# Optimization experiments

Hardware: AMD Instinct MI355X
Metric: run time of the kernel (lower is better)

The kernel has to match this reference:

```python
import jax, jax.numpy as jnp
import numpy as np

N = 25000
E = 400000
HIDDEN = 512
NH = 8
DH = HIDDEN // NH


def setup_inputs() -> dict:
    key = jax.random.key(0)
    ks = jax.random.split(key, 10)
    s = 1.0 / np.sqrt(HIDDEN)
    return {
        "h": jax.random.normal(ks[0], (N, HIDDEN), dtype=jnp.float32),
        "Wq": jax.random.normal(ks[1], (HIDDEN, HIDDEN), dtype=jnp.float32) * s,
        "bq": jnp.zeros((HIDDEN,), dtype=jnp.float32),
        "Wk": jax.random.normal(ks[2], (HIDDEN, HIDDEN), dtype=jnp.float32) * s,
        "bk": jnp.zeros((HIDDEN,), dtype=jnp.float32),
        "Wo": jax.random.normal(ks[3], (HIDDEN, HIDDEN), dtype=jnp.float32) * s,
        "bo": jnp.zeros((HIDDEN,), dtype=jnp.float32),
        "rows": jax.random.randint(ks[4], (E,), 0, N, dtype=jnp.int32),
        "cols": jax.random.randint(ks[5], (E,), 0, N, dtype=jnp.int32),
    }


def reference(h, Wq, bq, Wk, bk, Wo, bo, rows, cols):
    # Projections; reshape (N, dh, nh) exactly as the source does.
    q = (h @ Wq + bq).reshape(N, DH, NH)
    k = (h @ Wk + bk).reshape(N, DH, NH)
    v = k  # source bug kept faithfully: v = linear_k(h)

    # SDDMM: per-edge, per-head dot product (no 1/sqrt(dh) scaling in source).
    scores = jnp.einsum("edh,edh->eh", q[rows], k[cols])  # [E, NH]

    # Row-wise (source-node) segment softmax per head.
    m = jax.ops.segment_max(scores, rows, num_segments=N)       # [N, NH]
    ex = jnp.exp(scores - m[rows])                              # [E, NH]
    denom = jax.ops.segment_sum(ex, rows, num_segments=N)      # [N, NH]
    attn = ex / denom[rows]                                     # [E, NH]

    # SpMM: out[i] = sum_{j in nbr(i)} attn[ij] * v[j]
    msgs = attn[:, None, :] * v[cols]                           # [E, DH, NH]
    out = jax.ops.segment_sum(msgs, rows, num_segments=N)      # [N, DH, NH]

    return out.reshape(N, HIDDEN) @ Wo + bo
```

## Files before the change

### kernel.cpp

```cpp
#include <hip/hip_runtime.h>
#include <math.h>

typedef unsigned short u16;
typedef unsigned int u32;
typedef __attribute__((ext_vector_type(8))) _Float16 half8;
typedef __attribute__((ext_vector_type(2))) _Float16 half2v;
typedef __attribute__((ext_vector_type(8))) u16 ushort8;
typedef __attribute__((ext_vector_type(4))) float f32x4;

__device__ __forceinline__ u16 f2h(float f) {
    union { u16 u; _Float16 h; } c; c.h = (_Float16)f; return c.u;
}

#if __has_builtin(__builtin_amdgcn_fdot2)
#define FDOT2(a, b, c) __builtin_amdgcn_fdot2((a), (b), (c), false)
#else
#define FDOT2(a, b, c) fmaf((float)(a)[0], (float)(b)[0], \
                        fmaf((float)(a)[1], (float)(b)[1], (c)))
#endif

__device__ __forceinline__ void gload16(void* lds, const void* g) {
    __builtin_amdgcn_global_load_lds(
        (const __attribute__((address_space(1))) u32*)g,
        (__attribute__((address_space(3))) u32*)lds,
        16, 0, 0);
}

template <int OUTMODE>
__device__ __forceinline__ void gemm_body(
    const u16* A, const u16* Bt, const float* bias, void* Cout, int Mout,
    int m0, int n0, u16* As0, u16* As1, u16* Bs0, u16* Bs1)
{
    const int tid  = threadIdx.x;
    const int wave = tid >> 6;
    const int lane = tid & 63;
    const int wr = (wave >> 1) * 64;
    const int wc = (wave & 1) * 64;

    f32x4 acc[4][4];
#pragma unroll
    for (int i = 0; i < 4; ++i)
#pragma unroll
        for (int j = 0; j < 4; ++j) acc[i][j] = (f32x4){0.f, 0.f, 0.f, 0.f};

    const int srow  = lane >> 2;
    const int scolG = ((lane & 3) ^ ((srow >> 1) & 3)) * 8;
    const size_t gOffA = (size_t)(m0 + wave * 32 + srow) * 512 + scolG;
    const size_t gOffB = (size_t)(n0 + wave * 32 + srow) * 512 + scolG;
    const int lOff = wave * 1024 + srow * 32 + (lane & 3) * 8;

    const int fR = ((lane & 15) >> 1) & 3;
    const int paOff = (wr + (lane & 15)) * 32 + ((lane >> 4) ^ fR) * 8;
    const int pbOff = (wc + (lane & 15)) * 32 + ((lane >> 4) ^ fR) * 8;

    auto STAGE = [&](u16* sa, u16* sb, int ko) {
        gload16(sa + lOff,       A  + gOffA + ko);
        gload16(sa + lOff + 512, A  + gOffA + ko + 16 * 512);
        gload16(sb + lOff,       Bt + gOffB + ko);
        gload16(sb + lOff + 512, Bt + gOffB + ko + 16 * 512);
    };
    auto COMPUTE = [&](const u16* sa, const u16* sb) {
        half8 af[4], bf[4];
#pragma unroll
        for (int i = 0; i < 4; ++i) af[i] = *(const half8*)(sa + paOff + i * 512);
#pragma unroll
        for (int j = 0; j < 4; ++j) bf[j] = *(const half8*)(sb + pbOff + j * 512);
#pragma unroll
        for (int i = 0; i < 4; ++i)
#pragma unroll
            for (int j = 0; j < 4; ++j)
                acc[i][j] = __builtin_amdgcn_mfma_f32_16x16x32_f16(
                    af[i], bf[j], acc[i][j], 0, 0, 0);
    };

    STAGE(As0, Bs0, 0);
    __syncthreads();
#pragma unroll
    for (int kt = 0; kt < 16; kt += 2) {
        STAGE(As1, Bs1, (kt + 1) * 32);
        COMPUTE(As0, Bs0);
        __syncthreads();
        if (kt + 2 < 16) STAGE(As0, Bs0, (kt + 2) * 32);
        COMPUTE(As1, Bs1);
        __syncthreads();
    }

    const int ccol  = n0 + wc + (lane & 15);
    const int crow0 = m0 + wr + (lane >> 4) * 4;
#pragma unroll
    for (int j = 0; j < 4; ++j) {
        const float b = bias[ccol + j * 16];
#pragma unroll
        for (int i = 0; i < 4; ++i) {
#pragma unroll
            for (int r = 0; r < 4; ++r) {
                int row = crow0 + i * 16 + r;
                if (row < Mout) {
                    float v = acc[i][j][r] + b;
                    size_t off = (size_t)row * 512 + ccol + j * 16;
                    if (OUTMODE == 0) ((float*)Cout)[off] = v;
                    else              ((u16*)Cout)[off] = f2h(v);
                }
            }
        }
    }
}

__global__ __launch_bounds__(256) void gemm_qk(
    const u16* __restrict__ hh, const u16* __restrict__ Wqt,
    const u16* __restrict__ Wkt, const float* __restrict__ bqp,
    const float* __restrict__ bkp, u16* __restrict__ Qh,
    u16* __restrict__ Kb, int nPad)
{
    const int bid = blockIdx.x;
    const int m = (bid >> 6) * 8 + (bid & 7);
    const int s = (bid >> 3) & 7;
    if (m >= nPad / 128) return;
    const int z = s >> 2;
    const int n = s & 3;

    __shared__ __align__(16) u16 As0[4096], As1[4096], Bs0[4096], Bs1[4096];
    const u16* Bt = z ? Wkt : Wqt;
    const float* bias = z ? bkp : bqp;
    u16* out = z ? Kb : Qh;
    gemm_body<1>(hh, Bt, bias, out, nPad, m * 128, n * 128,
                 As0, As1, Bs0, Bs1);
}

__global__ __launch_bounds__(256) void gemm_wo(
    const u16* __restrict__ A, const u16* __restrict__ Wot,
    const float* __restrict__ bo, float* __restrict__ C, int Mout, int nPad)
{
    const int bid = blockIdx.x;
    const int m = (bid >> 5) * 8 + (bid & 7);
    const int s = (bid >> 3) & 3;
    if (m >= nPad / 128) return;

    __shared__ __align__(16) u16 As0[4096], As1[4096], Bs0[4096], Bs1[4096];
    gemm_body<0>(A, Wot, bo, C, Mout, m * 128, s * 128,
                 As0, As1, Bs0, Bs1);
}

__global__ __launch_bounds__(256) void prep(
    const float* __restrict__ h, u16* __restrict__ hh, int nN,
    const int* __restrict__ rows, int* __restrict__ deg, int E,
    const float* __restrict__ Wq, const float* __restrict__ Wk,
    const float* __restrict__ Wo, const float* __restrict__ bq,
    const float* __restrict__ bk,
    u16* __restrict__ Wqt, u16* __restrict__ Wkt, u16* __restrict__ Wot,
    float* __restrict__ bqp, float* __restrict__ bkp,
    int nbH, int nbE)
{
    __shared__ float T[64][65];
    const int tid = threadIdx.x;
    const int b = blockIdx.x;

    if (b < nbH) {
        int t = b * 256 + tid;
        size_t e = (size_t)t * 8;
        int row = (int)(e >> 9);
        ushort8 o;
        if (row < nN) {
            f32x4 a = *(const f32x4*)(h + e);
            f32x4 bb = *(const f32x4*)(h + e + 4);
            float x[8] = {a.x, a.y, a.z, a.w, bb.x, bb.y, bb.z, bb.w};
#pragma unroll
            for (int i = 0; i < 8; ++i) o[i] = f2h(x[i]);
        } else {
            o = (ushort8){0,0,0,0,0,0,0,0};
        }
        *(ushort8*)(hh + e) = o;
        return;
    }
    if (b < nbH + nbE) {
        int i = (b - nbH) * 256 + tid;
        if (i < E) atomicAdd(&deg[rows[i]], 1);
        return;
    }
    int rem = b - nbH - nbE;
    const int z = rem >> 6;
    const int X = (rem & 7) * 64;
    const int Y = ((rem >> 3) & 7) * 64;

    const int r4 = tid >> 4;
    const int c4 = (tid & 15) * 4;
    if (z < 2) {
        const float* W = z ? Wk : Wq;
#pragma unroll
        for (int rr = 0; rr < 64; rr += 16) {
            f32x4 v = *(const f32x4*)(W + (size_t)(X + rr + r4) * 512 + Y + c4);
            T[rr + r4][c4 + 0] = v.x; T[rr + r4][c4 + 1] = v.y;
            T[rr + r4][c4 + 2] = v.z; T[rr + r4][c4 + 3] = v.w;
        }
    } else {
#pragma unroll
        for (int rr = 0; rr < 64; rr += 16) {
            int p2 = (rr + r4) * 8 + (X >> 6);
            f32x4 v = *(const f32x4*)(Wo + (size_t)p2 * 512 + Y + c4);
            T[rr + r4][c4 + 0] = v.x; T[rr + r4][c4 + 1] = v.y;
            T[rr + r4][c4 + 2] = v.z; T[rr + r4][c4 + 3] = v.w;
        }
    }
    __syncthreads();

    const int cc = tid >> 2;
    const int ks = (tid & 3) * 16;
    const int pc = Y + cc;
    const int ro = (z < 2) ? ((pc & 7) * 64 + (pc >> 3)) : pc;
    ushort8 h0, h1;
#pragma unroll
    for (int t = 0; t < 8; ++t) {
        h0[t] = f2h(T[ks + t][cc]);
        h1[t] = f2h(T[ks + 8 + t][cc]);
    }
    size_t o = (size_t)ro * 512 + X + ks;
    if (z == 0) {
        *(ushort8*)(Wqt + o) = h0; *(ushort8*)(Wqt + o + 8) = h1;
    } else if (z == 1) {
        *(ushort8*)(Wkt + o) = h0; *(ushort8*)(Wkt + o + 8) = h1;
    } else {
        *(ushort8*)(Wot + o) = h0; *(ushort8*)(Wot + o + 8) = h1;
        if (rem == 128) {
            for (int bi = tid; bi < 512; bi += 256) {
                int pp = (bi & 63) * 8 + (bi >> 6);
                bqp[bi] = bq[pp];
                bkp[bi] = bk[pp];
            }
        }
    }
}

#define SCAN_CHUNK 2048

__global__ __launch_bounds__(256) void scan_partial(
    const int* __restrict__ deg, int* __restrict__ bsum, int n)
{
    int base = blockIdx.x * SCAN_CHUNK;
    int t = threadIdx.x;
    int s = 0;
    for (int i = t; i < SCAN_CHUNK; i += 256) {
        int g = base + i;
        s += (g < n) ? deg[g] : 0;
    }
#pragma unroll
    for (int off = 1; off < 64; off <<= 1) s += __shfl_xor(s, off, 64);
    __shared__ int ws[4];
    if ((t & 63) == 0) ws[t >> 6] = s;
    __syncthreads();
    if (t == 0) bsum[blockIdx.x] = ws[0] + ws[1] + ws[2] + ws[3];
}

__global__ __launch_bounds__(256) void scan_final(
    const int* __restrict__ deg, const int* __restrict__ bsum,
    int* __restrict__ rowptr, int* __restrict__ cursor, int n, int nb)
{
    int boff = 0, total = 0;
    for (int i = 0; i < nb; ++i) {
        int v = bsum[i];
        if (i < (int)blockIdx.x) boff += v;
        total += v;
    }
    int t = threadIdx.x;
    int base = blockIdx.x * SCAN_CHUNK + t * 8;
    int v[8];
    int s = 0;
#pragma unroll
    for (int i = 0; i < 8; ++i) {
        int g = base + i;
        v[i] = (g < n) ? deg[g] : 0;
        s += v[i];
    }
    int lane = t & 63, w = t >> 6;
    int inc = s;
#pragma unroll
    for (int off = 1; off < 64; off <<= 1) {
        int x = __shfl_up(inc, off, 64);
        if (lane >= off) inc += x;
    }
    __shared__ int wsum[4];
    if (lane == 63) wsum[w] = inc;
    __syncthreads();
    int excl = boff + inc - s;
    for (int i = 0; i < w; ++i) excl += wsum[i];
#pragma unroll
    for (int i = 0; i < 8; ++i) {
        int g = base + i;
        if (g < n) { rowptr[g] = excl; cursor[g] = excl; }
        excl += v[i];
    }
    if (blockIdx.x == 0 && t == 0) rowptr[n] = total;
}

__global__ void scatter_kernel(const int* __restrict__ rows, const int* __restrict__ cols,
                               int* __restrict__ cursor, int* __restrict__ colc, int E)
{
    int i = blockIdx.x * 256 + threadIdx.x;
    if (i < E) {
        int pos = atomicAdd(&cursor[rows[i]], 1);
        colc[pos] = cols[i];
    }
}

__global__ __launch_bounds__(256) void node_agg(
    const u16* __restrict__ Qh, const u16* __restrict__ Kb,
    const int* __restrict__ rowptr, const int* __restrict__ colc,
    u16* __restrict__ aggb, int nN)
{
    int node = blockIdx.x * 4 + (threadIdx.x >> 6);
    int lane = threadIdx.x & 63;
    if (node >= nN) return;
    size_t base = (size_t)node * 512 + lane * 8;

    half8 qv = __builtin_nontemporal_load((const half8*)(Qh + base));
    half2v q2[4];
#pragma unroll
    for (int i = 0; i < 4; ++i) q2[i] = (half2v){qv[2 * i], qv[2 * i + 1]};

    int start = rowptr[node];
    int deg   = rowptr[node + 1] - start;
    const int* cp = colc + start;
    const size_t loff = (size_t)lane * 8;

    float m = -__builtin_inff();
    float den = 0.f;
    half2v acc2[4];
#pragma unroll
    for (int i = 0; i < 4; ++i) acc2[i] = (half2v){(_Float16)0.f, (_Float16)0.f};

    if (deg > 0) {
        const int dl = deg - 1;
        half8 k0 = *(const half8*)(Kb + (size_t)cp[0] * 512 + loff);
        half8 k1 = *(const half8*)(Kb + (size_t)cp[1 < dl ? 1 : dl] * 512 + loff);
        half8 k2 = *(const half8*)(Kb + (size_t)cp[2 < dl ? 2 : dl] * 512 + loff);
        half8 k3 = *(const half8*)(Kb + (size_t)cp[3 < dl ? 3 : dl] * 512 + loff);
        for (int j = 0; j < deg; j += 4) {
            int i4 = j + 4 < dl ? j + 4 : dl;
            int i5 = j + 5 < dl ? j + 5 : dl;
            int i6 = j + 6 < dl ? j + 6 : dl;
            int i7 = j + 7 < dl ? j + 7 : dl;
            half8 n0 = *(const half8*)(Kb + (size_t)cp[i4] * 512 + loff);
            half8 n1 = *(const half8*)(Kb + (size_t)cp[i5] * 512 + loff);
            half8 n2 = *(const half8*)(Kb + (size_t)cp[i6] * 512 + loff);
            half8 n3 = *(const half8*)(Kb + (size_t)cp[i7] * 512 + loff);

            float p0 = 0.f, p1 = 0.f, p2 = 0.f, p3 = 0.f;
#pragma unroll
            for (int i = 0; i < 4; ++i) {
                half2v a = q2[i];
                half2v b0 = (half2v){k0[2 * i], k0[2 * i + 1]};
                half2v b1 = (half2v){k1[2 * i], k1[2 * i + 1]};
                half2v b2 = (half2v){k2[2 * i], k2[2 * i + 1]};
                half2v b3 = (half2v){k3[2 * i], k3[2 * i + 1]};
                p0 = FDOT2(a, b0, p0);
                p1 = FDOT2(a, b1, p1);
                p2 = FDOT2(a, b2, p2);
                p3 = FDOT2(a, b3, p3);
            }
#pragma unroll
            for (int off = 1; off < 8; off <<= 1) {
                p0 += __shfl_xor(p0, off, 64);
                p1 += __shfl_xor(p1, off, 64);
                p2 += __shfl_xor(p2, off, 64);
                p3 += __shfl_xor(p3, off, 64);
            }

            float pm = fmaxf(fmaxf(p0, p1), fmaxf(p2, p3));
            if (__any(pm > m + 4.f)) {
                float mn = fmaxf(m, pm);
                float sc = __expf(m - mn);
                den *= sc;
                _Float16 sch = (_Float16)sc;
                half2v sc2 = {sch, sch};
#pragma unroll
                for (int i = 0; i < 4; ++i) acc2[i] *= sc2;
                m = mn;
            }
            float w0 = __expf(p0 - m);
            float w1 = (j + 1 < deg) ? __expf(p1 - m) : 0.f;
            float w2 = (j + 2 < deg) ? __expf(p2 - m) : 0.f;
            float w3 = (j + 3 < deg) ? __expf(p3 - m) : 0.f;
            den += (w0 + w1) + (w2 + w3);
            _Float16 h0 = (_Float16)w0, h1 = (_Float16)w1;
            _Float16 h2 = (_Float16)w2, h3 = (_Float16)w3;
            half2v w02 = {h0, h0}, w12 = {h1, h1}, w22 = {h2, h2}, w32 = {h3, h3};
#pragma unroll
            for (int i = 0; i < 4; ++i) {
                half2v b0 = (half2v){k0[2 * i], k0[2 * i + 1]};
                half2v b1 = (half2v){k1[2 * i], k1[2 * i + 1]};
                half2v b2 = (half2v){k2[2 * i], k2[2 * i + 1]};
                half2v b3 = (half2v){k3[2 * i], k3[2 * i + 1]};
                acc2[i] += w02 * b0;
                acc2[i] += w12 * b1;
                acc2[i] += w22 * b2;
                acc2[i] += w32 * b3;
            }
            k0 = n0; k1 = n1; k2 = n2; k3 = n3;
        }
    }

    float inv = (deg > 0) ? 1.f / den : 0.f;
    ushort8 o;
#pragma unroll
    for (int i = 0; i < 4; ++i) {
        o[2 * i]     = f2h((float)acc2[i][0] * inv);
        o[2 * i + 1] = f2h((float)acc2[i][1] * inv);
    }
    __builtin_nontemporal_store(o, (ushort8*)(aggb + base));
}

extern "C" void kernel_launch(void* const* d_in, const int* in_sizes, int n_in,
                              void* d_out, int out_size, void* d_ws, size_t ws_size,
                              hipStream_t stream)
{
    const float* h  = (const float*)d_in[0];
    const float* Wq = (const float*)d_in[1];
    const float* bq = (const float*)d_in[2];
    const float* Wk = (const float*)d_in[3];
    const float* bk = (const float*)d_in[4];
    const float* Wo = (const float*)d_in[5];
    const float* bo = (const float*)d_in[6];
    const int* rows = (const int*)d_in[7];
    const int* cols = (const int*)d_in[8];
    float* out = (float*)d_out;

    const int HID = 512;
    const int nN  = in_sizes[0] / HID;
    const int E   = in_sizes[7];
    const int nPad = (nN + 127) & ~127;
    const int nb = (nN + SCAN_CHUNK - 1) / SCAN_CHUNK;
    const int nbH = nPad * (HID / 8) / 256;
    const int nbE = (E + 255) / 256;
    const int nMt = nPad / 128;
    const int nGrp = (nMt + 7) / 8;

    char* w = (char*)d_ws;
    u16* Kb  = (u16*)w;  w += (size_t)nPad * HID * 2;
    u16* hh  = (u16*)w;  w += (size_t)nPad * HID * 2;
    u16* Qh  = (u16*)w;  w += (size_t)nPad * HID * 2;
    u16* Wqt = (u16*)w;  w += 512 * 512 * 2;
    u16* Wkt = (u16*)w;  w += 512 * 512 * 2;
    u16* Wot = (u16*)w;  w += 512 * 512 * 2;
    float* bqp = (float*)w;  w += 512 * 4;
    float* bkp = (float*)w;  w += 512 * 4;
    int* rowptr = (int*)w;   w += (size_t)(nN + 1) * 4;
    int* cursor = (int*)w;   w += (size_t)nN * 4;
    int* deg    = (int*)w;   w += (size_t)nN * 4;
    int* bsum   = (int*)w;   w += 64 * 4;
    int* colc   = (int*)w;

    (void)hipMemsetAsync(deg, 0, (size_t)nN * sizeof(int), stream);

    prep<<<nbH + nbE + 192, 256, 0, stream>>>(
        h, hh, nN, rows, deg, E, Wq, Wk, Wo, bq, bk,
        Wqt, Wkt, Wot, bqp, bkp, nbH, nbE);

    scan_partial<<<nb, 256, 0, stream>>>(deg, bsum, nN);
    scan_final<<<nb, 256, 0, stream>>>(deg, bsum, rowptr, cursor, nN, nb);
    scatter_kernel<<<(E + 255) / 256, 256, 0, stream>>>(rows, cols, cursor, colc, E);

    gemm_qk<<<nGrp * 64, 256, 0, stream>>>(
        hh, Wqt, Wkt, bqp, bkp, Qh, Kb, nPad);

    node_agg<<<(nN + 3) / 4, 256, 0, stream>>>(Qh, Kb, rowptr, colc, hh, nN);

    gemm_wo<<<nGrp * 32, 256, 0, stream>>>(hh, Wot, bo, out, nN, nPad);
}
```

Baseline: 235.3 us.

## Widen GEMM tiles to 128x256 and deepen edge prefetch in node aggregation

The GEMM tile grows from 128x128 to 128x256 outputs per block. Each wave now holds a 4x8 MFMA accumulator, the B staging buffers double, and the grid shrinks by half. This aims to reuse A tiles across more columns and cut block count. Separately, the node aggregation loop now processes and prefetches 8 neighbor K rows per iteration instead of 4, to hide gather latency. The costs are higher register and LDS pressure, possible lower occupancy, and more wasted work for low-degree nodes.

```diff
diff --git a/kernel.cpp b/kernel.cpp
--- a/kernel.cpp
+++ b/kernel.cpp
@@ -28,47 +28,50 @@
 
 template <int OUTMODE>
 __device__ __forceinline__ void gemm_body(
-    const u16* A, const u16* Bt, const float* bias, void* Cout, int Mout,
-    int m0, int n0, u16* As0, u16* As1, u16* Bs0, u16* Bs1)
+    const u16* A, const u16* Bp, const float* bias, void* Cout, int Mout,
+    int m0, int colBase, u16* As0, u16* As1, u16* Bs0, u16* Bs1)
 {
     const int tid  = threadIdx.x;
     const int wave = tid >> 6;
     const int lane = tid & 63;
     const int wr = (wave >> 1) * 64;
-    const int wc = (wave & 1) * 64;
-
-    f32x4 acc[4][4];
+    const int wc = (wave & 1) * 128;
+
+    f32x4 acc[4][8];
 #pragma unroll
     for (int i = 0; i < 4; ++i)
 #pragma unroll
-        for (int j = 0; j < 4; ++j) acc[i][j] = (f32x4){0.f, 0.f, 0.f, 0.f};
+        for (int j = 0; j < 8; ++j) acc[i][j] = (f32x4){0.f, 0.f, 0.f, 0.f};
 
     const int srow  = lane >> 2;
     const int scolG = ((lane & 3) ^ ((srow >> 1) & 3)) * 8;
     const size_t gOffA = (size_t)(m0 + wave * 32 + srow) * 512 + scolG;
-    const size_t gOffB = (size_t)(n0 + wave * 32 + srow) * 512 + scolG;
-    const int lOff = wave * 1024 + srow * 32 + (lane & 3) * 8;
+    const size_t gOffB = (size_t)(wave * 64 + srow) * 512 + scolG;
+    const int lOffA = wave * 1024 + srow * 32 + (lane & 3) * 8;
+    const int lOffB = wave * 2048 + srow * 32 + (lane & 3) * 8;
 
     const int fR = ((lane & 15) >> 1) & 3;
     const int paOff = (wr + (lane & 15)) * 32 + ((lane >> 4) ^ fR) * 8;
     const int pbOff = (wc + (lane & 15)) * 32 + ((lane >> 4) ^ fR) * 8;
 
     auto STAGE = [&](u16* sa, u16* sb, int ko) {
-        gload16(sa + lOff,       A  + gOffA + ko);
-        gload16(sa + lOff + 512, A  + gOffA + ko + 16 * 512);
-        gload16(sb + lOff,       Bt + gOffB + ko);
-        gload16(sb + lOff + 512, Bt + gOffB + ko + 16 * 512);
+        gload16(sa + lOffA,        A  + gOffA + ko);
+        gload16(sa + lOffA + 512,  A  + gOffA + ko + 16 * 512);
+        gload16(sb + lOffB,        Bp + gOffB + ko);
+        gload16(sb + lOffB + 512,  Bp + gOffB + ko + 16 * 512);
+        gload16(sb + lOffB + 1024, Bp + gOffB + ko + 32 * 512);
+        gload16(sb + lOffB + 1536, Bp + gOffB + ko + 48 * 512);
     };
     auto COMPUTE = [&](const u16* sa, const u16* sb) {
-        half8 af[4], bf[4];
+        half8 af[4], bf[8];
 #pragma unroll
         for (int i = 0; i < 4; ++i) af[i] = *(const half8*)(sa + paOff + i * 512);
 #pragma unroll
-        for (int j = 0; j < 4; ++j) bf[j] = *(const half8*)(sb + pbOff + j * 512);
+        for (int j = 0; j < 8; ++j) bf[j] = *(const half8*)(sb + pbOff + j * 512);
 #pragma unroll
         for (int i = 0; i < 4; ++i)
 #pragma unroll
-            for (int j = 0; j < 4; ++j)
+            for (int j = 0; j < 8; ++j)
                 acc[i][j] = __builtin_amdgcn_mfma_f32_16x16x32_f16(
                     af[i], bf[j], acc[i][j], 0, 0, 0);
     };
@@ -85,11 +88,12 @@
         __syncthreads();
     }
 
-    const int ccol  = n0 + wc + (lane & 15);
+    const int ccolL = wc + (lane & 15);
     const int crow0 = m0 + wr + (lane >> 4) * 4;
 #pragma unroll
-    for (int j = 0; j < 4; ++j) {
-        const float b = bias[ccol + j * 16];
+    for (int j = 0; j < 8; ++j) {
+        const float b = bias[ccolL + j * 16];
+        const int col = colBase + ccolL + j * 16;
 #pragma unroll
         for (int i = 0; i < 4; ++i) {
 #pragma unroll
@@ -97,7 +101,7 @@
                 int row = crow0 + i * 16 + r;
                 if (row < Mout) {
                     float v = acc[i][j][r] + b;
-                    size_t off = (size_t)row * 512 + ccol + j * 16;
+                    size_t off = (size_t)row * 512 + col;
                     if (OUTMODE == 0) ((float*)Cout)[off] = v;
                     else              ((u16*)Cout)[off] = f2h(v);
                 }
@@ -113,18 +117,17 @@
     u16* __restrict__ Kb, int nPad)
 {
     const int bid = blockIdx.x;
-    const int m = (bid >> 6) * 8 + (bid & 7);
-    const int s = (bid >> 3) & 7;
+    const int m = (bid >> 5) * 8 + (bid & 7);
+    const int s = (bid >> 3) & 3;
     if (m >= nPad / 128) return;
-    const int z = s >> 2;
-    const int n = s & 3;
-
-    __shared__ __align__(16) u16 As0[4096], As1[4096], Bs0[4096], Bs1[4096];
-    const u16* Bt = z ? Wkt : Wqt;
-    const float* bias = z ? bkp : bqp;
+    const int z = s >> 1;
+    const int nloc = (s & 1) * 256;
+
+    __shared__ __align__(16) u16 As0[4096], As1[4096], Bs0[8192], Bs1[8192];
+    const u16* Bp = (z ? Wkt : Wqt) + (size_t)nloc * 512;
+    const float* bp = (z ? bkp : bqp) + nloc;
     u16* out = z ? Kb : Qh;
-    gemm_body<1>(hh, Bt, bias, out, nPad, m * 128, n * 128,
-                 As0, As1, Bs0, Bs1);
+    gemm_body<1>(hh, Bp, bp, out, nPad, m * 128, nloc, As0, As1, Bs0, Bs1);
 }
 
 __global__ __launch_bounds__(256) void gemm_wo(
@@ -132,13 +135,14 @@
     const float* __restrict__ bo, float* __restrict__ C, int Mout, int nPad)
 {
     const int bid = blockIdx.x;
-    const int m = (bid >> 5) * 8 + (bid & 7);
-    const int s = (bid >> 3) & 3;
+    const int m = (bid >> 4) * 8 + (bid & 7);
+    const int s = (bid >> 3) & 1;
     if (m >= nPad / 128) return;
-
-    __shared__ __align__(16) u16 As0[4096], As1[4096], Bs0[4096], Bs1[4096];
-    gemm_body<0>(A, Wot, bo, C, Mout, m * 128, s * 128,
-                 As0, As1, Bs0, Bs1);
+    const int nloc = s * 256;
+
+    __shared__ __align__(16) u16 As0[4096], As1[4096], Bs0[8192], Bs1[8192];
+    gemm_body<0>(A, Wot + (size_t)nloc * 512, bo + nloc, C, Mout,
+                 m * 128, nloc, As0, As1, Bs0, Bs1);
 }
 
 __global__ __launch_bounds__(256) void prep(
@@ -329,42 +333,40 @@
 
     if (deg > 0) {
         const int dl = deg - 1;
-        half8 k0 = *(const half8*)(Kb + (size_t)cp[0] * 512 + loff);
-        half8 k1 = *(const half8*)(Kb + (size_t)cp[1 < dl ? 1 : dl] * 512 + loff);
-        half8 k2 = *(const half8*)(Kb + (size_t)cp[2 < dl ? 2 : dl] * 512 + loff);
-        half8 k3 = *(const half8*)(Kb + (size_t)cp[3 < dl ? 3 : dl] * 512 + loff);
-        for (int j = 0; j < deg; j += 4) {
-            int i4 = j + 4 < dl ? j + 4 : dl;
-            int i5 = j + 5 < dl ? j + 5 : dl;
-            int i6 = j + 6 < dl ? j + 6 : dl;
-            int i7 = j + 7 < dl ? j + 7 : dl;
-            half8 n0 = *(const half8*)(Kb + (size_t)cp[i4] * 512 + loff);
-            half8 n1 = *(const half8*)(Kb + (size_t)cp[i5] * 512 + loff);
-            half8 n2 = *(const half8*)(Kb + (size_t)cp[i6] * 512 + loff);
-            half8 n3 = *(const half8*)(Kb + (size_t)cp[i7] * 512 + loff);
-
-            float p0 = 0.f, p1 = 0.f, p2 = 0.f, p3 = 0.f;
-#pragma unroll
-            for (int i = 0; i < 4; ++i) {
-                half2v a = q2[i];
-                half2v b0 = (half2v){k0[2 * i], k0[2 * i + 1]};
-                half2v b1 = (half2v){k1[2 * i], k1[2 * i + 1]};
-                half2v b2 = (half2v){k2[2 * i], k2[2 * i + 1]};
-                half2v b3 = (half2v){k3[2 * i], k3[2 * i + 1]};
-                p0 = FDOT2(a, b0, p0);
-                p1 = FDOT2(a, b1, p1);
-                p2 = FDOT2(a, b2, p2);
-                p3 = FDOT2(a, b3, p3);
+        half8 k[8];
+#pragma unroll
+        for (int t = 0; t < 8; ++t) {
+            int it = t < dl ? t : dl;
+            k[t] = *(const half8*)(Kb + (size_t)cp[it] * 512 + loff);
+        }
+        for (int j = 0; j < deg; j += 8) {
+            half8 nx[8];
+#pragma unroll
+            for (int t = 0; t < 8; ++t) {
+                int it = j + 8 + t < dl ? j + 8 + t : dl;
+                nx[t] = *(const half8*)(Kb + (size_t)cp[it] * 512 + loff);
+            }
+
+            float p[8];
+#pragma unroll
+            for (int t = 0; t < 8; ++t) {
+                float s = 0.f;
+#pragma unroll
+                for (int i = 0; i < 4; ++i) {
+                    half2v bb = (half2v){k[t][2 * i], k[t][2 * i + 1]};
+                    s = FDOT2(q2[i], bb, s);
+                }
+                p[t] = s;
             }
 #pragma unroll
             for (int off = 1; off < 8; off <<= 1) {
-                p0 += __shfl_xor(p0, off, 64);
-                p1 += __shfl_xor(p1, off, 64);
-                p2 += __shfl_xor(p2, off, 64);
-                p3 += __shfl_xor(p3, off, 64);
-            }
-
-            float pm = fmaxf(fmaxf(p0, p1), fmaxf(p2, p3));
+#pragma unroll
+                for (int t = 0; t < 8; ++t) p[t] += __shfl_xor(p[t], off, 64);
+            }
+
+            float pm = p[0];
+#pragma unroll
+            for (int t = 1; t < 8; ++t) pm = fmaxf(pm, p[t]);
             if (__any(pm > m + 4.f)) {
                 float mn = fmaxf(m, pm);
                 float sc = __expf(m - mn);
@@ -375,26 +377,20 @@
                 for (int i = 0; i < 4; ++i) acc2[i] *= sc2;
                 m = mn;
             }
-            float w0 = __expf(p0 - m);
-            float w1 = (j + 1 < deg) ? __expf(p1 - m) : 0.f;
-            float w2 = (j + 2 < deg) ? __expf(p2 - m) : 0.f;
-            float w3 = (j + 3 < deg) ? __expf(p3 - m) : 0.f;
-            den += (w0 + w1) + (w2 + w3);
-            _Float16 h0 = (_Float16)w0, h1 = (_Float16)w1;
-            _Float16 h2 = (_Float16)w2, h3 = (_Float16)w3;
-            half2v w02 = {h0, h0}, w12 = {h1, h1}, w22 = {h2, h2}, w32 = {h3, h3};
-#pragma unroll
-            for (int i = 0; i < 4; ++i) {
-                half2v b0 = (half2v){k0[2 * i], k0[2 * i + 1]};
-                half2v b1 = (half2v){k1[2 * i], k1[2 * i + 1]};
-                half2v b2 = (half2v){k2[2 * i], k2[2 * i + 1]};
-                half2v b3 = (half2v){k3[2 * i], k3[2 * i + 1]};
-                acc2[i] += w02 * b0;
-                acc2[i] += w12 * b1;
-                acc2[i] += w22 * b2;
-                acc2[i] += w32 * b3;
-            }
-            k0 = n0; k1 = n1; k2 = n2; k3 = n3;
+#pragma unroll
+            for (int t = 0; t < 8; ++t) {
+                float w = (j + t < deg) ? __expf(p[t] - m) : 0.f;
+                den += w;
+                _Float16 wh = (_Float16)w;
+                half2v w2 = {wh, wh};
+#pragma unroll
+                for (int i = 0; i < 4; ++i) {
+                    half2v bb = (half2v){k[t][2 * i], k[t][2 * i + 1]};
+                    acc2[i] += w2 * bb;
+                }
+            }
+#pragma unroll
+            for (int t = 0; t < 8; ++t) k[t] = nx[t];
         }
     }
 
@@ -458,10 +454,10 @@
     scan_final<<<nb, 256, 0, stream>>>(deg, bsum, rowptr, cursor, nN, nb);
     scatter_kernel<<<(E + 255) / 256, 256, 0, stream>>>(rows, cols, cursor, colc, E);
 
-    gemm_qk<<<nGrp * 64, 256, 0, stream>>>(
+    gemm_qk<<<nGrp * 32, 256, 0, stream>>>(
         hh, Wqt, Wkt, bqp, bkp, Qh, Kb, nPad);
 
     node_agg<<<(nN + 3) / 4, 256, 0, stream>>>(Qh, Kb, rowptr, colc, hh, nN);
 
-    gemm_wo<<<nGrp * 32, 256, 0, stream>>>(hh, Wot, bo, out, nN, nPad);
-}
+    gemm_wo<<<nGrp * 16, 256, 0, stream>>>(hh, Wot, bo, out, nN, nPad);
+}
```

Measured after the change: 233.6 us. About the same (-0.7%).
